# Performance work log

Hardware: AMD Instinct MI355X
Metric: run time of the kernel (lower is better)

Reference implementation:

```python
import jax, jax.numpy as jnp
import numpy as np

N0 = 4096
C = 128
DEPTH = 3
RATIO = 0.5
AVG_DEG = 32
BN_EPS = 1e-5


def setup_inputs() -> dict:
    key = jax.random.key(0)
    ks = jax.random.split(key, 6)
    x = jax.random.normal(ks[0], (N0, C), dtype=jnp.float32)
    # sparse symmetric adjacency (avg degree ~AVG_DEG), no self loops, dense layout
    mask = jax.random.bernoulli(ks[1], AVG_DEG / N0, (N0, N0)).astype(jnp.float32)
    adj = jnp.maximum(mask, mask.T) * (1.0 - jnp.eye(N0, dtype=jnp.float32))
    scale = 1.0 / np.sqrt(C)
    conv_w = jax.random.normal(ks[2], (2 * DEPTH + 1, C, C), dtype=jnp.float32) * scale
    conv_b = jax.random.normal(ks[3], (2 * DEPTH + 1, C), dtype=jnp.float32) * 0.01
    pool_w = jax.random.normal(ks[4], (DEPTH, C), dtype=jnp.float32)
    bn_g = jnp.ones((2 * DEPTH + 1, C), dtype=jnp.float32)
    bn_b = jnp.zeros((2 * DEPTH + 1, C), dtype=jnp.float32)
    return {"x": x, "adj": adj, "conv_w": conv_w, "conv_b": conv_b,
            "pool_w": pool_w, "bn_g": bn_g, "bn_b": bn_b}


def _gcn(x, A, W, b):
    # GCNConv(improved=True): A_hat = A + 2I, symmetric deg normalization
    n = A.shape[0]
    Ah = A + 2.0 * jnp.eye(n, dtype=A.dtype)
    deg = Ah.sum(axis=1)
    d_safe = jnp.where(deg > 0, deg, 1.0)
    dn = jnp.where(deg > 0, jax.lax.rsqrt(d_safe), 0.0)
    An = dn[:, None] * Ah * dn[None, :]
    return An @ (x @ W) + b


def _bn(x, g, b):
    # BatchNorm1d, training mode (biased variance)
    m = x.mean(axis=0)
    v = x.var(axis=0)
    return g * (x - m) * jax.lax.rsqrt(v + BN_EPS) + b


def _augment(A):
    # add_self_loops -> spspmm(A,A) -> remove_self_loops, done densely
    n = A.shape[0]
    I = jnp.eye(n, dtype=A.dtype)
    Aa = A + I
    return (Aa @ Aa) * (1.0 - I)


def _topk_pool(x, A, p):
    score = jnp.tanh((x @ p) / jnp.linalg.norm(p))
    k = int(np.ceil(RATIO * x.shape[0]))
    vals, perm = jax.lax.top_k(score, k)
    xn = x[perm] * vals[:, None]
    An = A[perm][:, perm]
    return xn, An, perm


def reference(x, adj, conv_w, conv_b, pool_w, bn_g, bn_b):
    x = x.astype(jnp.float32)
    x = _bn(jax.nn.relu(_gcn(x, adj, conv_w[0], conv_b[0])), bn_g[0], bn_b[0])
    xs, adjs, perms = [x], [adj], []
    A = adj
    for i in range(1, DEPTH + 1):
        A2 = _augment(A)
        x, A, perm = _topk_pool(x, A2, pool_w[i - 1])
        x = _bn(jax.nn.relu(_gcn(x, A, conv_w[i], conv_b[i])), bn_g[i], bn_b[i])
        if i < DEPTH:
            xs.append(x)
            adjs.append(A)
        perms.append(perm)
    for i in range(DEPTH):
        j = DEPTH - 1 - i
        res, Aj, perm = xs[j], adjs[j], perms[j]
        up = jnp.zeros_like(res).at[perm].set(x)
        x = res + up  # sum_res=True
        x = _gcn(x, Aj, conv_w[DEPTH + 1 + i], conv_b[DEPTH + 1 + i])
        if i < DEPTH - 1:
            x = jax.nn.relu(x)
        x = _bn(x, bn_g[DEPTH + 1 + i], bn_b[DEPTH + 1 + i])
    return x
```

## Files before the change

### kernel.cpp

```cpp
#include <hip/hip_runtime.h>
#include <cstdint>
#include <cstddef>

typedef __bf16 bf16;
typedef __bf16 bf16x8 __attribute__((ext_vector_type(8)));
typedef __bf16 bf16x4 __attribute__((ext_vector_type(4)));
typedef float floatx4 __attribute__((ext_vector_type(4)));
typedef int   intx4  __attribute__((ext_vector_type(4)));
typedef short shortx4 __attribute__((ext_vector_type(4)));
typedef char  cx8    __attribute__((ext_vector_type(8)));

#define GLD16(gp, lp) __builtin_amdgcn_global_load_lds( \
    (const __attribute__((address_space(1))) void*)(gp), \
    (__attribute__((address_space(3))) void*)(lp), 16, 0, 0)

__global__ __launch_bounds__(256) void gemm_sym_i8(
    const char* __restrict__ R, short* __restrict__ Cs16, int* __restrict__ Cs32,
    int n , int kIters, int G, int pairs)
{
  __shared__ __align__(16) char As[128 * 64];
  __shared__ __align__(16) char Bs[128 * 64];

  const int pair = blockIdx.x;
  int rem = pair, bm = 0;
  while (rem >= G - bm) { rem -= G - bm; ++bm; }
  const int bn = bm + rem;
  const int m0 = bm * 128;
  const int n0 = bn * 128;

  const int t = threadIdx.x;
  const int w = t >> 6, l = t & 63;
  const int wr = w >> 1, wc = w & 1;
  const int lr = l & 15, q = l >> 4;
  const int k0base = blockIdx.y * kIters * 64;

  const char* Ab = R + (size_t)m0 * n + k0base;
  const char* Bb = R + (size_t)n0 * n + k0base;
  const int srow = t >> 2;
  const int schunk = (t & 3) * 16;

  intx4 acc[4][4];
#pragma unroll
  for (int i = 0; i < 4; ++i)
#pragma unroll
    for (int j = 0; j < 4; ++j) acc[i][j] = (intx4)0;

  for (int kb = 0; kb < kIters; ++kb) {
    const int k0 = kb * 64;
    __syncthreads();
    GLD16(Ab + (size_t)srow * n + k0 + schunk,        As + (size_t)t * 16);
    GLD16(Ab + (size_t)(srow + 64) * n + k0 + schunk, As + (size_t)(t + 256) * 16);
    GLD16(Bb + (size_t)srow * n + k0 + schunk,        Bs + (size_t)t * 16);
    GLD16(Bb + (size_t)(srow + 64) * n + k0 + schunk, Bs + (size_t)(t + 256) * 16);
    __syncthreads();

    intx4 af[4], bfr[4];
#pragma unroll
    for (int mi = 0; mi < 4; ++mi)
      af[mi] = *(const intx4*)&As[(wr * 64 + mi * 16 + lr) * 64 + q * 16];
#pragma unroll
    for (int ni = 0; ni < 4; ++ni)
      bfr[ni] = *(const intx4*)&Bs[(wc * 64 + ni * 16 + lr) * 64 + q * 16];
#pragma unroll
    for (int mi = 0; mi < 4; ++mi)
#pragma unroll
      for (int ni = 0; ni < 4; ++ni)
        acc[mi][ni] = __builtin_amdgcn_mfma_i32_16x16x64_i8(
            af[mi], bfr[ni], acc[mi][ni], 0, 0, 0);
  }

  const size_t so = ((size_t)blockIdx.y * pairs + pair) * 16384;
#pragma unroll
  for (int mi = 0; mi < 4; ++mi)
#pragma unroll
    for (int ni = 0; ni < 4; ++ni) {
      const int cl = wc * 64 + ni * 16 + lr;
      const int rb = wr * 64 + mi * 16 + q * 4;
#pragma unroll
      for (int r = 0; r < 4; ++r) {
        int v = acc[mi][ni][r];
        if (Cs16) Cs16[so + (size_t)(rb + r) * 128 + cl] = (short)v;
        else      Cs32[so + (size_t)(rb + r) * 128 + cl] = v;
      }
    }
}

__global__ void sym_post_i(const short* __restrict__ Cs16, const int* __restrict__ Cs32,
                           bf16* __restrict__ Abf, float* __restrict__ Af,
                           int k, int G, int pairs, int nz)
{
  int rem = blockIdx.x, bm = 0;
  while (rem >= G - bm) { rem -= G - bm; ++bm; }
  const int bn = bm + rem;
  const int t = threadIdx.x;
  const int i = t >> 1;
  const int jc = blockIdx.y * 8 + (t & 1) * 4;
  const int r = bm * 128 + i;
  const size_t sbase = (size_t)blockIdx.x * 16384 + (size_t)i * 128 + jc;

  int v[4] = {0, 0, 0, 0};
  for (int z = 0; z < nz; ++z) {
    const size_t off = sbase + (size_t)z * pairs * 16384;
    if (Cs16) {
      shortx4 a = *(const shortx4*)&Cs16[off];
#pragma unroll
      for (int e = 0; e < 4; ++e) v[e] += (int)a[e];
    } else {
      intx4 a = *(const intx4*)&Cs32[off];
#pragma unroll
      for (int e = 0; e < 4; ++e) v[e] += a[e];
    }
  }
  const int c0 = bn * 128 + jc;
#pragma unroll
  for (int e = 0; e < 4; ++e)
    if (c0 + e == r) v[e] = 0;

  if (Abf) {
    bf16x4 o;
#pragma unroll
    for (int e = 0; e < 4; ++e) o[e] = (bf16)(float)v[e];
    *(bf16x4*)&Abf[(size_t)r * k + c0] = o;
    if (bm != bn) {
#pragma unroll
      for (int e = 0; e < 4; ++e)
        Abf[(size_t)(c0 + e) * k + r] = o[e];
    }
  } else {
    floatx4 o;
#pragma unroll
    for (int e = 0; e < 4; ++e) o[e] = (float)v[e];
    *(floatx4*)&Af[(size_t)r * k + c0] = o;
    if (bm != bn) {
#pragma unroll
      for (int e = 0; e < 4; ++e)
        Af[(size_t)(c0 + e) * k + r] = o[e];
    }
  }
}

__global__ __launch_bounds__(256) void gemm_sym(
    const bf16* __restrict__ R, float* __restrict__ CsF,
    int n , int kIters, int G, int pairs)
{
  __shared__ __align__(16) bf16 As[128 * 32];
  __shared__ __align__(16) bf16 Bs[128 * 32];

  const int pair = blockIdx.x;
  int rem = pair, bm = 0;
  while (rem >= G - bm) { rem -= G - bm; ++bm; }
  const int bn = bm + rem;
  const int m0 = bm * 128;
  const int n0 = bn * 128;

  const int t = threadIdx.x;
  const int w = t >> 6, l = t & 63;
  const int wr = w >> 1, wc = w & 1;
  const int lr = l & 15, q = l >> 4;
  const int k0base = blockIdx.y * kIters * 32;

  const bf16* Ab = R + (size_t)m0 * n + k0base;
  const bf16* Bb = R + (size_t)n0 * n + k0base;
  const int srow = t >> 2;
  const int schunk = (t & 3) * 8;

  floatx4 acc[4][4];
#pragma unroll
  for (int i = 0; i < 4; ++i)
#pragma unroll
    for (int j = 0; j < 4; ++j) acc[i][j] = (floatx4)0.0f;

  for (int kb = 0; kb < kIters; ++kb) {
    const int k0 = kb * 32;
    __syncthreads();
    GLD16(Ab + (size_t)srow * n + k0 + schunk,        As + (size_t)t * 8);
    GLD16(Ab + (size_t)(srow + 64) * n + k0 + schunk, As + (size_t)(t + 256) * 8);
    GLD16(Bb + (size_t)srow * n + k0 + schunk,        Bs + (size_t)t * 8);
    GLD16(Bb + (size_t)(srow + 64) * n + k0 + schunk, Bs + (size_t)(t + 256) * 8);
    __syncthreads();

    bf16x8 af[4], bfr[4];
#pragma unroll
    for (int mi = 0; mi < 4; ++mi)
      af[mi] = *(const bf16x8*)&As[(wr * 64 + mi * 16 + lr) * 32 + q * 8];
#pragma unroll
    for (int ni = 0; ni < 4; ++ni)
      bfr[ni] = *(const bf16x8*)&Bs[(wc * 64 + ni * 16 + lr) * 32 + q * 8];
#pragma unroll
    for (int mi = 0; mi < 4; ++mi)
#pragma unroll
      for (int ni = 0; ni < 4; ++ni)
        acc[mi][ni] = __builtin_amdgcn_mfma_f32_16x16x32_bf16(
            af[mi], bfr[ni], acc[mi][ni], 0, 0, 0);
  }

  const size_t so = ((size_t)blockIdx.y * pairs + pair) * 16384;
#pragma unroll
  for (int mi = 0; mi < 4; ++mi)
#pragma unroll
    for (int ni = 0; ni < 4; ++ni) {
      const int cl = wc * 64 + ni * 16 + lr;
      const int rb = wr * 64 + mi * 16 + q * 4;
#pragma unroll
      for (int r = 0; r < 4; ++r)
        CsF[so + (size_t)(rb + r) * 128 + cl] = acc[mi][ni][r];
    }
}

__global__ void sym_post(const float* __restrict__ CsF, float* __restrict__ Af,
                         int k, int G, int pairs, int nz)
{
  int rem = blockIdx.x, bm = 0;
  while (rem >= G - bm) { rem -= G - bm; ++bm; }
  const int bn = bm + rem;
  const int t = threadIdx.x;
  const int i = t >> 1;
  const int jc = blockIdx.y * 8 + (t & 1) * 4;
  const int r = bm * 128 + i;
  const size_t sbase = (size_t)blockIdx.x * 16384 + (size_t)i * 128 + jc;

  float v[4] = {0.f, 0.f, 0.f, 0.f};
  for (int z = 0; z < nz; ++z) {
    const size_t off = sbase + (size_t)z * pairs * 16384;
    floatx4 a = *(const floatx4*)&CsF[off];
#pragma unroll
    for (int e = 0; e < 4; ++e) v[e] += a[e];
  }
  const int c0 = bn * 128 + jc;
  floatx4 o;
#pragma unroll
  for (int e = 0; e < 4; ++e) o[e] = (c0 + e == r) ? 0.0f : v[e];
  *(floatx4*)&Af[(size_t)r * k + c0] = o;
  if (bm != bn) {
#pragma unroll
    for (int e = 0; e < 4; ++e)
      Af[(size_t)(c0 + e) * k + r] = o[e];
  }
}

template <int NP>
__global__ __launch_bounds__(256) void agg_bf(
    const bf16* __restrict__ A, int lda,
    const bf16* __restrict__ Zh, const bf16* __restrict__ Zm, const bf16* __restrict__ Zl,
    int ldz, float* __restrict__ Y, int kIters)
{
  __shared__ __align__(16) bf16 As[64 * 32];
  __shared__ __align__(16) bf16 Zs[NP][128 * 32];

  const int t = threadIdx.x;
  const int w = t >> 6, l = t & 63;
  const int wr = w >> 1, wc = w & 1;
  const int lr = l & 15, q = l >> 4;
  const int m0 = blockIdx.x * 64;
  const int k0base = blockIdx.y * kIters * 32;

  const int srow = t >> 2;
  const int schunk = (t & 3) * 8;

  floatx4 acc[2][4];
#pragma unroll
  for (int i = 0; i < 2; ++i)
#pragma unroll
    for (int j = 0; j < 4; ++j) acc[i][j] = (floatx4)0.0f;

  for (int kb = 0; kb < kIters; ++kb) {
    const int k0 = k0base + kb * 32;
    __syncthreads();
    GLD16(A + (size_t)(m0 + srow) * lda + k0 + schunk, As + (size_t)t * 8);
    GLD16(Zh + (size_t)srow * ldz + k0 + schunk,        Zs[0] + (size_t)t * 8);
    GLD16(Zh + (size_t)(srow + 64) * ldz + k0 + schunk, Zs[0] + (size_t)(t + 256) * 8);
    GLD16(Zm + (size_t)srow * ldz + k0 + schunk,        Zs[1] + (size_t)t * 8);
    GLD16(Zm + (size_t)(srow + 64) * ldz + k0 + schunk, Zs[1] + (size_t)(t + 256) * 8);
    if (NP > 2) {
      GLD16(Zl + (size_t)srow * ldz + k0 + schunk,        Zs[2] + (size_t)t * 8);
      GLD16(Zl + (size_t)(srow + 64) * ldz + k0 + schunk, Zs[2] + (size_t)(t + 256) * 8);
    }
    __syncthreads();

    bf16x8 af[2], bz[NP][4];
#pragma unroll
    for (int mi = 0; mi < 2; ++mi)
      af[mi] = *(const bf16x8*)&As[(wr * 32 + mi * 16 + lr) * 32 + q * 8];
#pragma unroll
    for (int s = 0; s < NP; ++s)
#pragma unroll
      for (int ni = 0; ni < 4; ++ni)
        bz[s][ni] = *(const bf16x8*)&Zs[s][(wc * 64 + ni * 16 + lr) * 32 + q * 8];
#pragma unroll
    for (int s = 0; s < NP; ++s)
#pragma unroll
      for (int mi = 0; mi < 2; ++mi)
#pragma unroll
        for (int ni = 0; ni < 4; ++ni)
          acc[mi][ni] = __builtin_amdgcn_mfma_f32_16x16x32_bf16(
              af[mi], bz[s][ni], acc[mi][ni], 0, 0, 0);
  }

#pragma unroll
  for (int mi = 0; mi < 2; ++mi)
#pragma unroll
    for (int ni = 0; ni < 4; ++ni) {
      const int col = wc * 64 + ni * 16 + lr;
      const int rowb = m0 + wr * 32 + mi * 16 + q * 4;
#pragma unroll
      for (int r = 0; r < 4; ++r)
        atomicAdd(&Y[(size_t)(rowb + r) * 128 + col], acc[mi][ni][r]);
    }
}

template <int NP>
__global__ __launch_bounds__(256) void agg_split(
    const float* __restrict__ A, int lda,
    const bf16* __restrict__ Zh, const bf16* __restrict__ Zm, const bf16* __restrict__ Zl,
    int ldz, float* __restrict__ Y, int kIters, int aTwo)
{
  __shared__ __align__(16) bf16 Ahs[64 * 32];
  __shared__ __align__(16) bf16 Als[64 * 32];
  __shared__ __align__(16) bf16 Zs[NP][128 * 32];

  const int t = threadIdx.x;
  const int w = t >> 6, l = t & 63;
  const int wr = w >> 1, wc = w & 1;
  const int lr = l & 15, q = l >> 4;
  const int m0 = blockIdx.x * 64;
  const int k0base = blockIdx.y * kIters * 32;

  const int arow = t >> 2;
  const int acol = (t & 3) * 8;
  const int srow = t >> 2;
  const int schunk = (t & 3) * 8;

  floatx4 acc[2][4];
#pragma unroll
  for (int i = 0; i < 2; ++i)
#pragma unroll
    for (int j = 0; j < 4; ++j) acc[i][j] = (floatx4)0.0f;

  for (int kb = 0; kb < kIters; ++kb) {
    const int k0 = k0base + kb * 32;
    const float* asrc = A + (size_t)(m0 + arow) * lda + k0 + acol;
    floatx4 av[2];
#pragma unroll
    for (int i = 0; i < 2; ++i) av[i] = *(const floatx4*)(asrc + i * 4);

    __syncthreads();
    GLD16(Zh + (size_t)srow * ldz + k0 + schunk,        Zs[0] + (size_t)t * 8);
    GLD16(Zh + (size_t)(srow + 64) * ldz + k0 + schunk, Zs[0] + (size_t)(t + 256) * 8);
    GLD16(Zm + (size_t)srow * ldz + k0 + schunk,        Zs[1] + (size_t)t * 8);
    GLD16(Zm + (size_t)(srow + 64) * ldz + k0 + schunk, Zs[1] + (size_t)(t + 256) * 8);
    if (NP > 2) {
      GLD16(Zl + (size_t)srow * ldz + k0 + schunk,        Zs[2] + (size_t)t * 8);
      GLD16(Zl + (size_t)(srow + 64) * ldz + k0 + schunk, Zs[2] + (size_t)(t + 256) * 8);
    }

    bf16x4 ah[2], alo[2];
    const int grow = m0 + arow;
#pragma unroll
    for (int i = 0; i < 8; ++i) {
      float v = av[i >> 2][i & 3];
      if (k0 + acol + i == grow) v = 0.0f;
      bf16 h = (bf16)v;
      ah[i >> 2][i & 3] = h;
      alo[i >> 2][i & 3] = (bf16)(v - (float)h);
    }
    const int sbase = arow * 32 + acol;
    *(bf16x4*)&Ahs[sbase] = ah[0]; *(bf16x4*)&Ahs[sbase + 4] = ah[1];
    if (aTwo) { *(bf16x4*)&Als[sbase] = alo[0]; *(bf16x4*)&Als[sbase + 4] = alo[1]; }
    __syncthreads();

    bf16x8 afh[2], afl[2], bz[NP][4];
#pragma unroll
    for (int mi = 0; mi < 2; ++mi)
      afh[mi] = *(const bf16x8*)&Ahs[(wr * 32 + mi * 16 + lr) * 32 + q * 8];
#pragma unroll
    for (int s = 0; s < NP; ++s)
#pragma unroll
      for (int ni = 0; ni < 4; ++ni)
        bz[s][ni] = *(const bf16x8*)&Zs[s][(wc * 64 + ni * 16 + lr) * 32 + q * 8];
#pragma unroll
    for (int s = 0; s < NP; ++s)
#pragma unroll
      for (int mi = 0; mi < 2; ++mi)
#pragma unroll
        for (int ni = 0; ni < 4; ++ni)
          acc[mi][ni] = __builtin_amdgcn_mfma_f32_16x16x32_bf16(
              afh[mi], bz[s][ni], acc[mi][ni], 0, 0, 0);
    if (aTwo) {
#pragma unroll
      for (int mi = 0; mi < 2; ++mi)
        afl[mi] = *(const bf16x8*)&Als[(wr * 32 + mi * 16 + lr) * 32 + q * 8];
      constexpr int NL = (NP > 2) ? 2 : 1;
#pragma unroll
      for (int s = 0; s < NL; ++s)
#pragma unroll
        for (int mi = 0; mi < 2; ++mi)
#pragma unroll
          for (int ni = 0; ni < 4; ++ni)
            acc[mi][ni] = __builtin_amdgcn_mfma_f32_16x16x32_bf16(
                afl[mi], bz[s][ni], acc[mi][ni], 0, 0, 0);
    }
  }

#pragma unroll
  for (int mi = 0; mi < 2; ++mi)
#pragma unroll
    for (int ni = 0; ni < 4; ++ni) {
      const int col = wc * 64 + ni * 16 + lr;
      const int rowb = m0 + wr * 32 + mi * 16 + q * 4;
#pragma unroll
      for (int r = 0; r < 4; ++r)
        atomicAdd(&Y[(size_t)(rowb + r) * 128 + col], acc[mi][ni][r]);
    }
}

template <int FULL>
__global__ __launch_bounds__(256) void xw_split(
    const float* __restrict__ X, const int* __restrict__ perm,
    const float* __restrict__ vals,
    const float* __restrict__ up, const int* __restrict__ inv,
    const float* __restrict__ statsP, const float* __restrict__ gP,
    const float* __restrict__ bP, float nP,
    const bf16* __restrict__ Wh, const bf16* __restrict__ Wm, const bf16* __restrict__ Wl,
    const float* __restrict__ dnv, float* __restrict__ Z,
    bf16* __restrict__ Zht, bf16* __restrict__ Zmt, bf16* __restrict__ Zlt, int ldz,
    float* __restrict__ Agg, float* __restrict__ stats)
{
  __shared__ __align__(16) bf16 Xs[3][128 * 32];
  __shared__ __align__(16) bf16 Ws[3][128 * 32];
  __shared__ float scU[128], offU[128];

  const int t = threadIdx.x;
  if (blockIdx.x == 0) stats[t] = 0.0f;

  const int w = t >> 6, l = t & 63;
  const int wr = w >> 1, wc = w & 1;
  const int lr = l & 15, q = l >> 4;
  const int r0 = blockIdx.x * 128;

  const int srow = t >> 1;
  const int soff = (t & 1) * 16;
  const int sbase = srow * 32 + soff;

  if (statsP) {
    if (t < 128) {
      float m = statsP[t] / nP;
      float var = statsP[128 + t] / nP - m * m;
      float sc = gP[t] / sqrtf(var + 1e-5f);
      scU[t] = sc;
      offU[t] = bP[t] - m * sc;
    }
    __syncthreads();
  }

  const int row = r0 + srow;
  int grow = row;
  float scale = 1.0f;
  if (perm) { grow = perm[row]; scale = vals[row]; }
  const float* xrow = X + (size_t)grow * 128;
  const float* uprow = nullptr;
  if (up) { int j = inv[row]; if (j >= 0) uprow = up + (size_t)j * 128; }

  floatx4 acc[4][4];
#pragma unroll
  for (int i = 0; i < 4; ++i)
#pragma unroll
    for (int j = 0; j < 4; ++j) acc[i][j] = (floatx4)0.0f;

  const bf16* wsrc[3] = {Wh, Wm, Wl};

  for (int ks = 0; ks < 4; ++ks) {
    const int k0 = ks * 32;
    float xv[16];
#pragma unroll
    for (int i = 0; i < 16; i += 4) {
      floatx4 tmp = *(const floatx4*)(xrow + k0 + soff + i);
      if (uprow) {
        floatx4 u = *(const floatx4*)(uprow + k0 + soff + i);
        if (statsP) {
#pragma unroll
          for (int j = 0; j < 4; ++j) {
            const int c = k0 + soff + i + j;
            u[j] = scU[c] * u[j] + offU[c];
          }
        }
        tmp += u;
      }
      xv[i] = tmp[0] * scale; xv[i + 1] = tmp[1] * scale;
      xv[i + 2] = tmp[2] * scale; xv[i + 3] = tmp[3] * scale;
    }
    bf16x8 wv[3][2];
#pragma unroll
    for (int s = 0; s < 3; ++s) {
      const bf16* ws = wsrc[s] + (size_t)srow * 128 + k0 + soff;
      wv[s][0] = *(const bf16x8*)ws;
      wv[s][1] = *(const bf16x8*)(ws + 8);
    }
    bf16x8 vh[2], vm[2], vl[2];
#pragma unroll
    for (int i = 0; i < 16; ++i) {
      float v = xv[i];
      bf16 h = (bf16)v; float r1 = v - (float)h;
      bf16 m = (bf16)r1; float r2 = r1 - (float)m;
      vh[i >> 3][i & 7] = h; vm[i >> 3][i & 7] = m; vl[i >> 3][i & 7] = (bf16)r2;
    }
    __syncthreads();
    *(bf16x8*)&Xs[0][sbase] = vh[0]; *(bf16x8*)&Xs[0][sbase + 8] = vh[1];
    *(bf16x8*)&Xs[1][sbase] = vm[0]; *(bf16x8*)&Xs[1][sbase + 8] = vm[1];
    *(bf16x8*)&Xs[2][sbase] = vl[0]; *(bf16x8*)&Xs[2][sbase + 8] = vl[1];
#pragma unroll
    for (int s = 0; s < 3; ++s) {
      *(bf16x8*)&Ws[s][sbase] = wv[s][0];
      *(bf16x8*)&Ws[s][sbase + 8] = wv[s][1];
    }
    __syncthreads();

    bf16x8 af[3][4], bfg[3][4];
#pragma unroll
    for (int s = 0; s < 3; ++s) {
#pragma unroll
      for (int mi = 0; mi < 4; ++mi)
        af[s][mi] = *(const bf16x8*)&Xs[s][(wr * 64 + mi * 16 + lr) * 32 + q * 8];
#pragma unroll
      for (int ni = 0; ni < 4; ++ni)
        bfg[s][ni] = *(const bf16x8*)&Ws[s][(wc * 64 + ni * 16 + lr) * 32 + q * 8];
    }
    constexpr int NT = FULL ? 6 : 3;
    constexpr int sa[6] = {0, 0, 1, 1, 0, 2};
    constexpr int sb[6] = {0, 1, 0, 1, 2, 0};
#pragma unroll
    for (int p = 0; p < NT; ++p)
#pragma unroll
      for (int mi = 0; mi < 4; ++mi)
#pragma unroll
        for (int ni = 0; ni < 4; ++ni)
          acc[mi][ni] = __builtin_amdgcn_mfma_f32_16x16x32_bf16(
              af[sa[p]][mi], bfg[sb[p]][ni], acc[mi][ni], 0, 0, 0);
  }

#pragma unroll
  for (int mi = 0; mi < 4; ++mi) {
    const int rowb = r0 + wr * 64 + mi * 16 + q * 4;
    float dnr[4];
#pragma unroll
    for (int r = 0; r < 4; ++r) dnr[r] = dnv[rowb + r];
#pragma unroll
    for (int ni = 0; ni < 4; ++ni) {
      const int col = wc * 64 + ni * 16 + lr;
      bf16x4 h4, m4, l4;
#pragma unroll
      for (int r = 0; r < 4; ++r) {
        float v = dnr[r] * acc[mi][ni][r];
        Z[(size_t)(rowb + r) * 128 + col] = v;
        Agg[(size_t)(rowb + r) * 128 + col] = 0.0f;
        bf16 h = (bf16)v; float r1 = v - (float)h;
        bf16 m = (bf16)r1; float r2 = r1 - (float)m;
        h4[r] = h; m4[r] = m; l4[r] = (bf16)r2;
      }
      *(bf16x4*)&Zht[(size_t)col * ldz + rowb] = h4;
      *(bf16x4*)&Zmt[(size_t)col * ldz + rowb] = m4;
      if (FULL) *(bf16x4*)&Zlt[(size_t)col * ldz + rowb] = l4;
    }
  }
}

__global__ void prep_all(const float* __restrict__ adj, bf16* __restrict__ ah,
                         float* __restrict__ dn, int n,
                         const float* __restrict__ W, bf16* __restrict__ Wh,
                         bf16* __restrict__ Wm, bf16* __restrict__ Wl,
                         const float* __restrict__ pw, float* __restrict__ invp) {
  const int bid = blockIdx.x;
  const int t = threadIdx.x;
  if (bid < 4096) {
    int r = bid;
    const float* arow = adj + (size_t)r * n;
    bf16* orow = ah + (size_t)r * n;
    float sum = 0.f;
    for (int c4 = t * 4; c4 < n; c4 += 1024) {
      floatx4 v = *(const floatx4*)(arow + c4);
      bf16x4 o;
#pragma unroll
      for (int e = 0; e < 4; ++e) {
        float x = (c4 + e == r) ? 0.0f : v[e];
        sum += x; o[e] = (bf16)x;
      }
      *(bf16x4*)&orow[c4] = o;
    }
    __shared__ float red[256];
    red[t] = sum; __syncthreads();
    for (int off = 128; off; off >>= 1) {
      if (t < off) red[t] += red[t + off];
      __syncthreads();
    }
    if (t == 0) dn[r] = 1.0f / sqrtf(red[0] + 2.0f);
  } else if (bid < 4544) {
    int idx = (bid - 4096) * 256 + t;
    int l = idx >> 14, rem = idx & 16383, c = rem >> 7, k = rem & 127;
    float v = W[(l << 14) + (k << 7) + c];
    bf16 h = (bf16)v; float r1 = v - (float)h;
    bf16 m = (bf16)r1; float r2 = r1 - (float)m;
    Wh[idx] = h; Wm[idx] = m; Wl[idx] = (bf16)r2;
  } else {
    __shared__ float red[128];
    if (t < 128) {
      for (int l = 0; l < 3; ++l) {
        float v = pw[l * 128 + t];
        red[t] = v * v; __syncthreads();
        for (int off = 64; off; off >>= 1) {
          if (t < off) red[t] += red[t + off];
          __syncthreads();
        }
        if (t == 0) invp[l] = 1.0f / sqrtf(red[0]);
        __syncthreads();
      }
    }
  }
}

__global__ void dn_rows_bf(const bf16* __restrict__ A, int lda, float* __restrict__ dn,
                           int n) {
  int r = blockIdx.x, t = threadIdx.x;
  const bf16* row = A + (size_t)r * lda;
  float sum = 0.f;
  for (int c4 = t * 4; c4 < n; c4 += 1024) {
    bf16x4 v = *(const bf16x4*)&row[c4];
#pragma unroll
    for (int e = 0; e < 4; ++e) sum += (float)v[e];
  }
  __shared__ float red[256];
  red[t] = sum; __syncthreads();
  for (int off = 128; off; off >>= 1) {
    if (t < off) red[t] += red[t + off];
    __syncthreads();
  }
  if (t == 0) dn[r] = 1.0f / sqrtf(red[0] + 2.0f);
}

__global__ void dn_rows(const float* __restrict__ A, int lda, float* __restrict__ dn,
                        int n) {
  int r = blockIdx.x, t = threadIdx.x;
  const float* row = A + (size_t)r * lda;
  float sum = 0.f;
  for (int c = t; c < n; c += 256)
    if (c != r) sum += row[c];
  __shared__ float red[256];
  red[t] = sum; __syncthreads();
  for (int off = 128; off; off >>= 1) {
    if (t < off) red[t] += red[t + off];
    __syncthreads();
  }
  if (t == 0) dn[r] = 1.0f / sqrtf(red[0] + 2.0f);
}

__device__ inline unsigned f2u(float f) {
  unsigned u = __float_as_uint(f);
  return (u & 0x80000000u) ? ~u : (u | 0x80000000u);
}
__global__ __launch_bounds__(1024) void select_kernel(
    const float* __restrict__ s, int n, int k,
    int* __restrict__ perm, float* __restrict__ vals, int* __restrict__ inv)
{
  __shared__ int hist[256];
  __shared__ unsigned sh_prefix;
  __shared__ int sh_krem;
  __shared__ float sh_thr;
  __shared__ int wsum[16];
  __shared__ int wgs[16], wes[16];
  const int t = threadIdx.x;
  const int lane = t & 63;
  const int wid = t >> 6;
  if (t == 0) { sh_prefix = 0; sh_krem = k; }

  for (int round = 0; round < 4; ++round) {
    const int shift = 24 - 8 * round;
    if (t < 256) hist[t] = 0;
    __syncthreads();
    const unsigned pref = sh_prefix;
    const int krem = sh_krem;
    for (int i = t; i < n; i += 1024) {
      unsigned u = f2u(s[i]);
      if (round == 0 || (u >> (shift + 8)) == pref)
        atomicAdd(&hist[(u >> shift) & 255], 1);
    }
    __syncthreads();
    int v = 0, own = 0;
    if (t < 256) {
      own = hist[255 - t];
      v = own;
#pragma unroll
      for (int off = 1; off < 64; off <<= 1) {
        int u = __shfl_up(v, off, 64);
        if (lane >= off) v += u;
      }
      if (lane == 63) wsum[wid] = v;
    }
    __syncthreads();
    if (t < 256) {
      int add = 0;
      for (int wi = 0; wi < wid; ++wi) add += wsum[wi];
      v += add;
      const int prev = v - own;
      if (v >= krem && prev < krem) {
        sh_prefix = (pref << 8) | (unsigned)(255 - t);
        sh_krem = krem - prev;
      }
    }
    __syncthreads();
  }
  if (t == 0) {
    unsigned u = sh_prefix;
    sh_thr = (u & 0x80000000u) ? __uint_as_float(u & 0x7fffffffu)
                               : __uint_as_float(~u);
  }
  for (int i = t; i < n; i += 1024) inv[i] = -1;
  __syncthreads();

  const float thr = sh_thr;
  const int chunk = n >> 10;
  const int beg = t * chunk;
  int g = 0, e = 0;
  for (int i = 0; i < chunk; ++i) {
    float v = s[beg + i];
    g += (v > thr); e += (v == thr);
  }
  int vg = g, ve = e;
#pragma unroll
  for (int off = 1; off < 64; off <<= 1) {
    int ug = __shfl_up(vg, off, 64);
    int ue = __shfl_up(ve, off, 64);
    if (lane >= off) { vg += ug; ve += ue; }
  }
  if (lane == 63) { wgs[wid] = vg; wes[wid] = ve; }
  __syncthreads();
  int ag = 0, ae = 0;
  for (int wi = 0; wi < wid; ++wi) { ag += wgs[wi]; ae += wes[wi]; }
  int total_gt = 0;
#pragma unroll
  for (int wi = 0; wi < 16; ++wi) total_gt += wgs[wi];
  int pg = vg + ag - g;
  int pe = ve + ae - e;
  const int need = k - total_gt;
  for (int i = 0; i < chunk; ++i) {
    float v = s[beg + i];
    if (v > thr) {
      if (pg < k) { perm[pg] = beg + i; vals[pg] = v; inv[beg + i] = pg; }
      ++pg;
    } else if (v == thr) {
      if (pe < need && total_gt + pe < k) {
        perm[total_gt + pe] = beg + i; vals[total_gt + pe] = v;
        inv[beg + i] = total_gt + pe;
      }
      ++pe;
    }
  }
}

__global__ void gather_i8(const bf16* __restrict__ src, int lda,
                          const int* __restrict__ perm, char* __restrict__ R, int n) {
  int j = blockIdx.x, t = threadIdx.x;
  int r = perm[j];
  const bf16* s = src + (size_t)r * lda;
  char* o = R + (size_t)j * n;
  for (int c = t * 8; c < n; c += 2048) {
    bf16x8 v = *(const bf16x8*)&s[c];
    cx8 ob;
#pragma unroll
    for (int e = 0; e < 8; ++e)
      ob[e] = (c + e == r) ? (char)1 : (char)(float)v[e];
    *(cx8*)&o[c] = ob;
  }
}

__global__ void gather_f32(const float* __restrict__ src, int lda,
                           const int* __restrict__ perm, bf16* __restrict__ R, int n) {
  int j = blockIdx.x, t = threadIdx.x;
  int r = perm[j];
  const float* s = src + (size_t)r * lda;
  bf16* o = R + (size_t)j * n;
  for (int c4 = t * 4; c4 < n; c4 += 1024) {
    floatx4 v = *(const floatx4*)(s + c4);
    bf16x4 ob;
#pragma unroll
    for (int e = 0; e < 4; ++e)
      ob[e] = (c4 + e == r) ? (bf16)1.0f : (bf16)v[e];
    *(bf16x4*)&o[c4] = ob;
  }
}

__global__ void gcn_post(float* __restrict__ acc, const float* __restrict__ Zf,
                         const float* __restrict__ dn, const float* __restrict__ bias,
                         float* __restrict__ stats, int relu,
                         float* __restrict__ hout) {
  int c = threadIdx.x;
  int r0 = blockIdx.x * 16;
  float b = bias[c];
  float s = 0.f, qq = 0.f;
  for (int i = 0; i < 16; ++i) {
    int r = r0 + i;
    float v = dn[r] * (acc[(size_t)r * 128 + c] + 2.0f * Zf[(size_t)r * 128 + c]) + b;
    if (relu) v = fmaxf(v, 0.f);
    hout[(size_t)r * 128 + c] = v;
    s += v; qq += v * v;
  }
  atomicAdd(&stats[c], s);
  atomicAdd(&stats[128 + c], qq);
}

__global__ void bn_apply(const float* __restrict__ H, const float* __restrict__ stats,
                         const float* __restrict__ g, const float* __restrict__ b,
                         int n, float* __restrict__ xout,
                         const float* __restrict__ pw, const float* __restrict__ invp,
                         float* __restrict__ scores) {
  int r = blockIdx.x, c = threadIdx.x;
  float m = stats[c] / n;
  float var = stats[128 + c] / n - m * m;
  float sc = g[c] / sqrtf(var + 1e-5f);
  float off = b[c] - m * sc;
  float v = sc * H[(size_t)r * 128 + c] + off;
  xout[(size_t)r * 128 + c] = v;
  if (pw) {
    __shared__ float red[128];
    red[c] = v * pw[c]; __syncthreads();
    for (int o = 64; o; o >>= 1) {
      if (c < o) red[c] += red[c + o];
      __syncthreads();
    }
    if (c == 0) scores[r] = tanhf(red[0] * invp[0]);
  }
}

extern "C" void kernel_launch(void* const* d_in, const int* in_sizes, int n_in,
                              void* d_out, int out_size, void* d_ws, size_t ws_size,
                              hipStream_t stream) {
  const float* x_in   = (const float*)d_in[0];
  const float* adj    = (const float*)d_in[1];
  const float* conv_w = (const float*)d_in[2];
  const float* conv_b = (const float*)d_in[3];
  const float* pool_w = (const float*)d_in[4];
  const float* bn_g   = (const float*)d_in[5];
  const float* bn_b   = (const float*)d_in[6];
  float* out = (float*)d_out;
  (void)in_sizes; (void)n_in; (void)out_size; (void)ws_size;

  char* p = (char*)d_ws;
  auto alloc = [&](size_t bytes) -> void* {
    void* r = (void*)p;
    p += (bytes + 255) & ~(size_t)255;
    return r;
  };
  bf16*  Ah0bf = (bf16*)alloc(4096ull * 4096 * 2);
  bf16*  A1bf  = (bf16*)alloc(2048ull * 2048 * 2);
  float* A2f   = (float*)alloc(1024ull * 1024 * 4);
  float* A3f   = (float*)alloc(512ull * 512 * 4);
  char*  Rbuf  = (char*)alloc(2048ull * 4096 * 2);
  void*  Cs    = alloc(40ull << 20);
  float* Z     = (float*)alloc(4096ull * 128 * 4);
  bf16*  Zht   = (bf16*)alloc(128ull * 4096 * 2);
  bf16*  Zmt   = (bf16*)alloc(128ull * 4096 * 2);
  bf16*  Zlt   = (bf16*)alloc(128ull * 4096 * 2);
  float* Agg   = (float*)alloc(4096ull * 128 * 4);
  float* res0  = (float*)alloc(4096ull * 128 * 4);
  float* res1  = (float*)alloc(2048ull * 128 * 4);
  float* res2  = (float*)alloc(1024ull * 128 * 4);
  float* xb0   = (float*)alloc(512ull * 128 * 4);
  float* xb1   = (float*)alloc(1024ull * 128 * 4);
  float* xb2   = (float*)alloc(2048ull * 128 * 4);
  bf16*  Wh    = (bf16*)alloc(7ull * 16384 * 2);
  bf16*  Wm    = (bf16*)alloc(7ull * 16384 * 2);
  bf16*  Wl    = (bf16*)alloc(7ull * 16384 * 2);
  float* scores = (float*)alloc(4096 * 4);
  int*   perm0 = (int*)alloc(2048 * 4);
  int*   perm1 = (int*)alloc(1024 * 4);
  int*   perm2 = (int*)alloc(512 * 4);
  int*   inv0  = (int*)alloc(4096 * 4);
  int*   inv1  = (int*)alloc(2048 * 4);
  int*   inv2  = (int*)alloc(1024 * 4);
  float* vals0 = (float*)alloc(2048 * 4);
  float* vals1 = (float*)alloc(1024 * 4);
  float* vals2 = (float*)alloc(512 * 4);
  float* dn0   = (float*)alloc(4096 * 4);
  float* dn1   = (float*)alloc(2048 * 4);
  float* dn2   = (float*)alloc(1024 * 4);
  float* dn3   = (float*)alloc(512 * 4);
  float* invp  = (float*)alloc(256);
  float* stats = (float*)alloc(7ull * 256 * 4);

  auto gcn = [&](int nr, const bf16* Abf, const float* Af32, const float* dnv,
                 int layer, const float* xsrc, const int* perm, const float* vals,
                 const float* up, const int* inv, float* xout, int relu, int aTwo,
                 const float* pw, const float* ip, int full,
                 const float* statsP, const float* gP, const float* bPv, float nP,
                 int doBn) {
    float* st = stats + layer * 256;
    if (full)
      xw_split<1><<<nr / 128, 256, 0, stream>>>(
          xsrc, perm, vals, up, inv, statsP, gP, bPv, nP,
          Wh + layer * 16384, Wm + layer * 16384, Wl + layer * 16384, dnv,
          Z, Zht, Zmt, Zlt, nr, Agg, st);
    else
      xw_split<0><<<nr / 128, 256, 0, stream>>>(
          xsrc, perm, vals, up, inv, statsP, gP, bPv, nP,
          Wh + layer * 16384, Wm + layer * 16384, Wl + layer * 16384, dnv,
          Z, Zht, Zmt, Zlt, nr, Agg, st);
    if (Abf) {
      if (full)
        agg_bf<3><<<dim3(nr / 64, 8), 256, 0, stream>>>(
            Abf, nr, Zht, Zmt, Zlt, nr, Agg, nr / 256);
      else
        agg_bf<2><<<dim3(nr / 64, 8), 256, 0, stream>>>(
            Abf, nr, Zht, Zmt, Zlt, nr, Agg, nr / 256);
    } else {
      if (full)
        agg_split<3><<<dim3(nr / 64, 8), 256, 0, stream>>>(
            Af32, nr, Zht, Zmt, Zlt, nr, Agg, nr / 256, aTwo);
      else
        agg_split<2><<<dim3(nr / 64, 8), 256, 0, stream>>>(
            Af32, nr, Zht, Zmt, Zlt, nr, Agg, nr / 256, aTwo);
    }
    gcn_post<<<nr / 16, 128, 0, stream>>>(Agg, Z, dnv, conv_b + layer * 128, st, relu,
                                          doBn ? Agg : xout);
    if (doBn)
      bn_apply<<<nr, 128, 0, stream>>>(Agg, st, bn_g + layer * 128, bn_b + layer * 128,
                                       nr, xout, pw, ip, scores);
  };

  auto pool = [&](int n, const bf16* srcBf, const float* srcF32,
                  bf16* outBf, float* outF32, float* dnNew,
                  int* perm, float* vals, int* inv, int splitZ, int mode) {
    int k = n / 2, G = k / 128, pairs = G * (G + 1) / 2;
    select_kernel<<<1, 1024, 0, stream>>>(scores, n, k, perm, vals, inv);
    if (mode <= 1) {
      gather_i8<<<k, 256, 0, stream>>>(srcBf, n, perm, Rbuf, n);
      gemm_sym_i8<<<dim3(pairs, splitZ), 256, 0, stream>>>(
          Rbuf, mode == 0 ? (short*)Cs : nullptr, mode == 0 ? nullptr : (int*)Cs,
          n, n / (splitZ * 64), G, pairs);
      sym_post_i<<<dim3(pairs, 16), 256, 0, stream>>>(
          mode == 0 ? (const short*)Cs : nullptr, mode == 0 ? nullptr : (const int*)Cs,
          outBf, outF32, k, G, pairs, splitZ);
    } else {
      gather_f32<<<k, 256, 0, stream>>>(srcF32, n, perm, (bf16*)Rbuf, n);
      gemm_sym<<<dim3(pairs, splitZ), 256, 0, stream>>>(
          (const bf16*)Rbuf, (float*)Cs, n, n / (splitZ * 32), G, pairs);
      sym_post<<<dim3(pairs, 16), 256, 0, stream>>>(
          (const float*)Cs, outF32, k, G, pairs, splitZ);
    }
    if (outBf) dn_rows_bf<<<k, 256, 0, stream>>>(outBf, k, dnNew, k);
    else       dn_rows<<<k, 256, 0, stream>>>(outF32, k, dnNew, k);
  };

  prep_all<<<4545, 256, 0, stream>>>(adj, Ah0bf, dn0, 4096,
                                     conv_w, Wh, Wm, Wl, pool_w, invp);

  gcn(4096, Ah0bf, nullptr, dn0, 0, x_in, nullptr, nullptr, nullptr, nullptr,
      res0, 1, 0, pool_w + 0, invp + 0, 1, nullptr, nullptr, nullptr, 1.0f, 1);
  pool(4096, Ah0bf, nullptr, A1bf, nullptr, dn1, perm0, vals0, inv0, 4, 0);
  gcn(2048, A1bf, nullptr, dn1, 1, res0, perm0, vals0, nullptr, nullptr,
      res1, 1, 0, pool_w + 128, invp + 1, 1, nullptr, nullptr, nullptr, 1.0f, 1);
  pool(2048, A1bf, nullptr, nullptr, A2f, dn2, perm1, vals1, inv1, 8, 1);
  gcn(1024, nullptr, A2f, dn2, 2, res1, perm1, vals1, nullptr, nullptr,
      res2, 1, 1, pool_w + 256, invp + 2, 1, nullptr, nullptr, nullptr, 1.0f, 1);
  pool(1024, nullptr, A2f, nullptr, A3f, dn3, perm2, vals2, inv2, 8, 2);
  gcn(512, nullptr, A3f, dn3, 3, res2, perm2, vals2, nullptr, nullptr,
      xb0, 1, 1, nullptr, nullptr, 0, nullptr, nullptr, nullptr, 1.0f, 0);

  gcn(1024, nullptr, A2f, dn2, 4, res2, nullptr, nullptr, xb0, inv2,
      xb1, 1, 1, nullptr, nullptr, 0,
      stats + 3 * 256, bn_g + 3 * 128, bn_b + 3 * 128, 512.0f, 0);
  gcn(2048, A1bf, nullptr, dn1, 5, res1, nullptr, nullptr, xb1, inv1,
      xb2, 1, 0, nullptr, nullptr, 0,
      stats + 4 * 256, bn_g + 4 * 128, bn_b + 4 * 128, 1024.0f, 0);
  gcn(4096, Ah0bf, nullptr, dn0, 6, res0, nullptr, nullptr, xb2, inv0,
      out, 0, 0, nullptr, nullptr, 0,
      stats + 5 * 256, bn_g + 5 * 128, bn_b + 5 * 128, 2048.0f, 1);
}
```

Measured before the change: 502.4 us.

## Use sparse neighbor-list aggregation for level-0 GCN and deterministic split-K reductions

Builds a capped neighbor list (up to 256 uint16 indices per row) for the original adjacency in prep_all and uses a gather-sum kernel for the two 4096-node GCN aggregations, replacing dense 4096x4096 bf16 MFMA products. Dense aggregations now write per-split partial outputs that gcn_post sums, instead of using atomicAdd. BN statistics switch to fixed-point int64 atomics so results are deterministic. This cuts most of the dense work at the largest level. The cost is extra partial-buffer traffic, and rows with more than 256 neighbors would be silently truncated.

```diff
diff --git a/kernel.cpp b/kernel.cpp
--- a/kernel.cpp
+++ b/kernel.cpp
@@ -13,6 +13,9 @@
 #define GLD16(gp, lp) __builtin_amdgcn_global_load_lds( \
     (const __attribute__((address_space(1))) void*)(gp), \
     (__attribute__((address_space(3))) void*)(lp), 16, 0, 0)
+
+#define FXS 16777216.0f
+#define FXI 5.9604644775390625e-08
 
 __global__ __launch_bounds__(256) void gemm_sym_i8(
     const char* __restrict__ R, short* __restrict__ Cs16, int* __restrict__ Cs32,
@@ -238,6 +241,35 @@
   }
 }
 
+__global__ __launch_bounds__(256) void agg_sparse(
+    const unsigned short* __restrict__ nbr, const int* __restrict__ deg,
+    const float* __restrict__ Z, float* __restrict__ Y)
+{
+  const int r = blockIdx.x * 4 + (threadIdx.x >> 6);
+  const int l = threadIdx.x & 63;
+  const unsigned short* rn = nbr + (size_t)r * 256;
+  const int d = deg[r];
+  float a0 = 0.f, a1 = 0.f;
+  int i = 0;
+  for (; i + 4 <= d; i += 4) {
+    const int c0 = rn[i], c1 = rn[i + 1], c2 = rn[i + 2], c3 = rn[i + 3];
+    float2 v0 = *(const float2*)(Z + (size_t)c0 * 128 + l * 2);
+    float2 v1 = *(const float2*)(Z + (size_t)c1 * 128 + l * 2);
+    float2 v2 = *(const float2*)(Z + (size_t)c2 * 128 + l * 2);
+    float2 v3 = *(const float2*)(Z + (size_t)c3 * 128 + l * 2);
+    a0 += v0.x; a1 += v0.y;
+    a0 += v1.x; a1 += v1.y;
+    a0 += v2.x; a1 += v2.y;
+    a0 += v3.x; a1 += v3.y;
+  }
+  for (; i < d; ++i) {
+    const int c = rn[i];
+    float2 v = *(const float2*)(Z + (size_t)c * 128 + l * 2);
+    a0 += v.x; a1 += v.y;
+  }
+  *(float2*)(Y + (size_t)r * 128 + l * 2) = make_float2(a0, a1);
+}
+
 template <int NP>
 __global__ __launch_bounds__(256) void agg_bf(
     const bf16* __restrict__ A, int lda,
@@ -296,6 +328,7 @@
               af[mi], bz[s][ni], acc[mi][ni], 0, 0, 0);
   }
 
+  const size_t zoff = (size_t)blockIdx.y * lda;
 #pragma unroll
   for (int mi = 0; mi < 2; ++mi)
 #pragma unroll
@@ -304,7 +337,7 @@
       const int rowb = m0 + wr * 32 + mi * 16 + q * 4;
 #pragma unroll
       for (int r = 0; r < 4; ++r)
-        atomicAdd(&Y[(size_t)(rowb + r) * 128 + col], acc[mi][ni][r]);
+        Y[(zoff + rowb + r) * 128 + col] = acc[mi][ni][r];
     }
 }
 
@@ -401,6 +434,7 @@
     }
   }
 
+  const size_t zoff = (size_t)blockIdx.y * lda;
 #pragma unroll
   for (int mi = 0; mi < 2; ++mi)
 #pragma unroll
@@ -409,7 +443,7 @@
       const int rowb = m0 + wr * 32 + mi * 16 + q * 4;
 #pragma unroll
       for (int r = 0; r < 4; ++r)
-        atomicAdd(&Y[(size_t)(rowb + r) * 128 + col], acc[mi][ni][r]);
+        Y[(zoff + rowb + r) * 128 + col] = acc[mi][ni][r];
     }
 }
 
@@ -418,19 +452,19 @@
     const float* __restrict__ X, const int* __restrict__ perm,
     const float* __restrict__ vals,
     const float* __restrict__ up, const int* __restrict__ inv,
-    const float* __restrict__ statsP, const float* __restrict__ gP,
+    const long long* __restrict__ statsP, const float* __restrict__ gP,
     const float* __restrict__ bP, float nP,
     const bf16* __restrict__ Wh, const bf16* __restrict__ Wm, const bf16* __restrict__ Wl,
     const float* __restrict__ dnv, float* __restrict__ Z,
     bf16* __restrict__ Zht, bf16* __restrict__ Zmt, bf16* __restrict__ Zlt, int ldz,
-    float* __restrict__ Agg, float* __restrict__ stats)
+    long long* __restrict__ stats)
 {
   __shared__ __align__(16) bf16 Xs[3][128 * 32];
   __shared__ __align__(16) bf16 Ws[3][128 * 32];
   __shared__ float scU[128], offU[128];
 
   const int t = threadIdx.x;
-  if (blockIdx.x == 0) stats[t] = 0.0f;
+  if (blockIdx.x == 0) stats[t] = 0;
 
   const int w = t >> 6, l = t & 63;
   const int wr = w >> 1, wc = w & 1;
@@ -443,8 +477,10 @@
 
   if (statsP) {
     if (t < 128) {
-      float m = statsP[t] / nP;
-      float var = statsP[128 + t] / nP - m * m;
+      float sm = (float)((double)statsP[t] * FXI);
+      float sq = (float)((double)statsP[128 + t] * FXI);
+      float m = sm / nP;
+      float var = sq / nP - m * m;
       float sc = gP[t] / sqrtf(var + 1e-5f);
       scU[t] = sc;
       offU[t] = bP[t] - m * sc;
@@ -551,47 +587,76 @@
       for (int r = 0; r < 4; ++r) {
         float v = dnr[r] * acc[mi][ni][r];
         Z[(size_t)(rowb + r) * 128 + col] = v;
-        Agg[(size_t)(rowb + r) * 128 + col] = 0.0f;
         bf16 h = (bf16)v; float r1 = v - (float)h;
         bf16 m = (bf16)r1; float r2 = r1 - (float)m;
         h4[r] = h; m4[r] = m; l4[r] = (bf16)r2;
       }
-      *(bf16x4*)&Zht[(size_t)col * ldz + rowb] = h4;
-      *(bf16x4*)&Zmt[(size_t)col * ldz + rowb] = m4;
-      if (FULL) *(bf16x4*)&Zlt[(size_t)col * ldz + rowb] = l4;
+      if (Zht) {
+        *(bf16x4*)&Zht[(size_t)col * ldz + rowb] = h4;
+        *(bf16x4*)&Zmt[(size_t)col * ldz + rowb] = m4;
+        if (FULL) *(bf16x4*)&Zlt[(size_t)col * ldz + rowb] = l4;
+      }
     }
   }
 }
 
 __global__ void prep_all(const float* __restrict__ adj, bf16* __restrict__ ah,
                          float* __restrict__ dn, int n,
+                         unsigned short* __restrict__ nbr, int* __restrict__ deg,
                          const float* __restrict__ W, bf16* __restrict__ Wh,
                          bf16* __restrict__ Wm, bf16* __restrict__ Wl,
                          const float* __restrict__ pw, float* __restrict__ invp) {
   const int bid = blockIdx.x;
   const int t = threadIdx.x;
+  __shared__ int wsum4[4];
+  __shared__ float red[128];
   if (bid < 4096) {
-    int r = bid;
+    const int r = bid;
     const float* arow = adj + (size_t)r * n;
     bf16* orow = ah + (size_t)r * n;
-    float sum = 0.f;
-    for (int c4 = t * 4; c4 < n; c4 += 1024) {
-      floatx4 v = *(const floatx4*)(arow + c4);
+    const int base = t * 16;
+    floatx4 buf[4];
+#pragma unroll
+    for (int i = 0; i < 4; ++i) buf[i] = *(const floatx4*)(arow + base + i * 4);
+    int cnt = 0;
+#pragma unroll
+    for (int i = 0; i < 4; ++i) {
       bf16x4 o;
 #pragma unroll
       for (int e = 0; e < 4; ++e) {
-        float x = (c4 + e == r) ? 0.0f : v[e];
-        sum += x; o[e] = (bf16)x;
+        float x = (base + i * 4 + e == r) ? 0.0f : buf[i][e];
+        buf[i][e] = x;
+        cnt += (x != 0.0f) ? 1 : 0;
+        o[e] = (bf16)x;
       }
-      *(bf16x4*)&orow[c4] = o;
-    }
-    __shared__ float red[256];
-    red[t] = sum; __syncthreads();
-    for (int off = 128; off; off >>= 1) {
-      if (t < off) red[t] += red[t + off];
-      __syncthreads();
-    }
-    if (t == 0) dn[r] = 1.0f / sqrtf(red[0] + 2.0f);
+      *(bf16x4*)&orow[base + i * 4] = o;
+    }
+    const int lane = t & 63, wid = t >> 6;
+    int vc = cnt;
+#pragma unroll
+    for (int off = 1; off < 64; off <<= 1) {
+      int u = __shfl_up(vc, off, 64);
+      if (lane >= off) vc += u;
+    }
+    if (lane == 63) wsum4[wid] = vc;
+    __syncthreads();
+    int add = 0;
+    for (int wi = 0; wi < wid; ++wi) add += wsum4[wi];
+    int o = vc + add - cnt;
+    const int total = wsum4[0] + wsum4[1] + wsum4[2] + wsum4[3];
+    unsigned short* rn = nbr + (size_t)r * 256;
+#pragma unroll
+    for (int i = 0; i < 4; ++i)
+#pragma unroll
+      for (int e = 0; e < 4; ++e)
+        if (buf[i][e] != 0.0f) {
+          if (o < 256) rn[o] = (unsigned short)(base + i * 4 + e);
+          ++o;
+        }
+    if (t == 0) {
+      deg[r] = total < 256 ? total : 256;
+      dn[r] = 1.0f / sqrtf((float)total + 2.0f);
+    }
   } else if (bid < 4544) {
     int idx = (bid - 4096) * 256 + t;
     int l = idx >> 14, rem = idx & 16383, c = rem >> 7, k = rem & 127;
@@ -600,7 +665,6 @@
     bf16 m = (bf16)r1; float r2 = r1 - (float)m;
     Wh[idx] = h; Wm[idx] = m; Wl[idx] = (bf16)r2;
   } else {
-    __shared__ float red[128];
     if (t < 128) {
       for (int l = 0; l < 3; ++l) {
         float v = pw[l * 128 + t];
@@ -786,33 +850,40 @@
   }
 }
 
-__global__ void gcn_post(float* __restrict__ acc, const float* __restrict__ Zf,
+__global__ void gcn_post(const float* Ys, const float* __restrict__ Zf,
                          const float* __restrict__ dn, const float* __restrict__ bias,
-                         float* __restrict__ stats, int relu,
-                         float* __restrict__ hout) {
+                         long long* __restrict__ stats, int relu,
+                         float* hout, int nr, int nz) {
   int c = threadIdx.x;
   int r0 = blockIdx.x * 16;
   float b = bias[c];
   float s = 0.f, qq = 0.f;
   for (int i = 0; i < 16; ++i) {
     int r = r0 + i;
-    float v = dn[r] * (acc[(size_t)r * 128 + c] + 2.0f * Zf[(size_t)r * 128 + c]) + b;
+    float a = 0.f;
+    for (int z = 0; z < nz; ++z)
+      a += Ys[((size_t)z * nr + r) * 128 + c];
+    float v = dn[r] * (a + 2.0f * Zf[(size_t)r * 128 + c]) + b;
     if (relu) v = fmaxf(v, 0.f);
     hout[(size_t)r * 128 + c] = v;
     s += v; qq += v * v;
   }
-  atomicAdd(&stats[c], s);
-  atomicAdd(&stats[128 + c], qq);
-}
-
-__global__ void bn_apply(const float* __restrict__ H, const float* __restrict__ stats,
+  atomicAdd((unsigned long long*)&stats[c],
+            (unsigned long long)(long long)llrintf(s * FXS));
+  atomicAdd((unsigned long long*)&stats[128 + c],
+            (unsigned long long)(long long)llrintf(qq * FXS));
+}
+
+__global__ void bn_apply(const float* __restrict__ H, const long long* __restrict__ stats,
                          const float* __restrict__ g, const float* __restrict__ b,
                          int n, float* __restrict__ xout,
                          const float* __restrict__ pw, const float* __restrict__ invp,
                          float* __restrict__ scores) {
   int r = blockIdx.x, c = threadIdx.x;
-  float m = stats[c] / n;
-  float var = stats[128 + c] / n - m * m;
+  float sm = (float)((double)stats[c] * FXI);
+  float sq = (float)((double)stats[128 + c] * FXI);
+  float m = sm / n;
+  float var = sq / n - m * m;
   float sc = g[c] / sqrtf(var + 1e-5f);
   float off = b[c] - m * sc;
   float v = sc * H[(size_t)r * 128 + c] + off;
@@ -857,7 +928,7 @@
   bf16*  Zht   = (bf16*)alloc(128ull * 4096 * 2);
   bf16*  Zmt   = (bf16*)alloc(128ull * 4096 * 2);
   bf16*  Zlt   = (bf16*)alloc(128ull * 4096 * 2);
-  float* Agg   = (float*)alloc(4096ull * 128 * 4);
+  float* Agg   = (float*)alloc(8ull * 2048 * 128 * 4);
   float* res0  = (float*)alloc(4096ull * 128 * 4);
   float* res1  = (float*)alloc(2048ull * 128 * 4);
   float* res2  = (float*)alloc(1024ull * 128 * 4);
@@ -867,6 +938,8 @@
   bf16*  Wh    = (bf16*)alloc(7ull * 16384 * 2);
   bf16*  Wm    = (bf16*)alloc(7ull * 16384 * 2);
   bf16*  Wl    = (bf16*)alloc(7ull * 16384 * 2);
+  unsigned short* nbr = (unsigned short*)alloc(4096ull * 256 * 2 + 1024);
+  int*   deg   = (int*)alloc(4096 * 4);
   float* scores = (float*)alloc(4096 * 4);
   int*   perm0 = (int*)alloc(2048 * 4);
   int*   perm1 = (int*)alloc(1024 * 4);
@@ -882,32 +955,41 @@
   float* dn2   = (float*)alloc(1024 * 4);
   float* dn3   = (float*)alloc(512 * 4);
   float* invp  = (float*)alloc(256);
-  float* stats = (float*)alloc(7ull * 256 * 4);
-
-  auto gcn = [&](int nr, const bf16* Abf, const float* Af32, const float* dnv,
+  long long* stats = (long long*)alloc(7ull * 256 * 8);
+
+  auto gcn = [&](int nr, const bf16* Abf, const float* Af32,
+                 const unsigned short* nbrp, const float* dnv,
                  int layer, const float* xsrc, const int* perm, const float* vals,
                  const float* up, const int* inv, float* xout, int relu, int aTwo,
                  const float* pw, const float* ip, int full,
-                 const float* statsP, const float* gP, const float* bPv, float nP,
+                 const long long* statsP, const float* gP, const float* bPv, float nP,
                  int doBn) {
-    float* st = stats + layer * 256;
+    long long* st = stats + layer * 256;
+    bf16* zht = nbrp ? nullptr : Zht;
+    bf16* zmt = nbrp ? nullptr : Zmt;
+    bf16* zlt = nbrp ? nullptr : Zlt;
     if (full)
       xw_split<1><<<nr / 128, 256, 0, stream>>>(
           xsrc, perm, vals, up, inv, statsP, gP, bPv, nP,
           Wh + layer * 16384, Wm + layer * 16384, Wl + layer * 16384, dnv,
-          Z, Zht, Zmt, Zlt, nr, Agg, st);
+          Z, zht, zmt, zlt, nr, st);
     else
       xw_split<0><<<nr / 128, 256, 0, stream>>>(
           xsrc, perm, vals, up, inv, statsP, gP, bPv, nP,
           Wh + layer * 16384, Wm + layer * 16384, Wl + layer * 16384, dnv,
-          Z, Zht, Zmt, Zlt, nr, Agg, st);
-    if (Abf) {
+          Z, zht, zmt, zlt, nr, st);
+    int nz;
+    if (nbrp) {
+      agg_sparse<<<nr / 4, 256, 0, stream>>>(nbrp, deg, Z, Agg);
+      nz = 1;
+    } else if (Abf) {
       if (full)
         agg_bf<3><<<dim3(nr / 64, 8), 256, 0, stream>>>(
             Abf, nr, Zht, Zmt, Zlt, nr, Agg, nr / 256);
       else
         agg_bf<2><<<dim3(nr / 64, 8), 256, 0, stream>>>(
             Abf, nr, Zht, Zmt, Zlt, nr, Agg, nr / 256);
+      nz = 8;
     } else {
       if (full)
         agg_split<3><<<dim3(nr / 64, 8), 256, 0, stream>>>(
@@ -915,9 +997,10 @@
       else
         agg_split<2><<<dim3(nr / 64, 8), 256, 0, stream>>>(
             Af32, nr, Zht, Zmt, Zlt, nr, Agg, nr / 256, aTwo);
+      nz = 8;
     }
     gcn_post<<<nr / 16, 128, 0, stream>>>(Agg, Z, dnv, conv_b + layer * 128, st, relu,
-                                          doBn ? Agg : xout);
+                                          doBn ? Agg : xout, nr, nz);
     if (doBn)
       bn_apply<<<nr, 128, 0, stream>>>(Agg, st, bn_g + layer * 128, bn_b + layer * 128,
                                        nr, xout, pw, ip, scores);
@@ -947,28 +1030,28 @@
     else       dn_rows<<<k, 256, 0, stream>>>(outF32, k, dnNew, k);
   };
 
-  prep_all<<<4545, 256, 0, stream>>>(adj, Ah0bf, dn0, 4096,
+  prep_all<<<4545, 256, 0, stream>>>(adj, Ah0bf, dn0, 4096, nbr, deg,
                                      conv_w, Wh, Wm, Wl, pool_w, invp);
 
-  gcn(4096, Ah0bf, nullptr, dn0, 0, x_in, nullptr, nullptr, nullptr, nullptr,
+  gcn(4096, nullptr, nullptr, nbr, dn0, 0, x_in, nullptr, nullptr, nullptr, nullptr,
       res0, 1, 0, pool_w + 0, invp + 0, 1, nullptr, nullptr, nullptr, 1.0f, 1);
   pool(4096, Ah0bf, nullptr, A1bf, nullptr, dn1, perm0, vals0, inv0, 4, 0);
-  gcn(2048, A1bf, nullptr, dn1, 1, res0, perm0, vals0, nullptr, nullptr,
+  gcn(2048, A1bf, nullptr, nullptr, dn1, 1, res0, perm0, vals0, nullptr, nullptr,
       res1, 1, 0, pool_w + 128, invp + 1, 1, nullptr, nullptr, nullptr, 1.0f, 1);
   pool(2048, A1bf, nullptr, nullptr, A2f, dn2, perm1, vals1, inv1, 8, 1);
-  gcn(1024, nullptr, A2f, dn2, 2, res1, perm1, vals1, nullptr, nullptr,
+  gcn(1024, nullptr, A2f, nullptr, dn2, 2, res1, perm1, vals1, nullptr, nullptr,
       res2, 1, 1, pool_w + 256, invp + 2, 1, nullptr, nullptr, nullptr, 1.0f, 1);
   pool(1024, nullptr, A2f, nullptr, A3f, dn3, perm2, vals2, inv2, 8, 2);
-  gcn(512, nullptr, A3f, dn3, 3, res2, perm2, vals2, nullptr, nullptr,
+  gcn(512, nullptr, A3f, nullptr, dn3, 3, res2, perm2, vals2, nullptr, nullptr,
       xb0, 1, 1, nullptr, nullptr, 0, nullptr, nullptr, nullptr, 1.0f, 0);
 
-  gcn(1024, nullptr, A2f, dn2, 4, res2, nullptr, nullptr, xb0, inv2,
+  gcn(1024, nullptr, A2f, nullptr, dn2, 4, res2, nullptr, nullptr, xb0, inv2,
       xb1, 1, 1, nullptr, nullptr, 0,
       stats + 3 * 256, bn_g + 3 * 128, bn_b + 3 * 128, 512.0f, 0);
-  gcn(2048, A1bf, nullptr, dn1, 5, res1, nullptr, nullptr, xb1, inv1,
+  gcn(2048, A1bf, nullptr, nullptr, dn1, 5, res1, nullptr, nullptr, xb1, inv1,
       xb2, 1, 0, nullptr, nullptr, 0,
       stats + 4 * 256, bn_g + 4 * 128, bn_b + 4 * 128, 1024.0f, 0);
-  gcn(4096, Ah0bf, nullptr, dn0, 6, res0, nullptr, nullptr, xb2, inv0,
+  gcn(4096, nullptr, nullptr, nbr, dn0, 6, res0, nullptr, nullptr, xb2, inv0,
       out, 0, 0, nullptr, nullptr, 0,
       stats + 5 * 256, bn_g + 5 * 128, bn_b + 5 * 128, 2048.0f, 1);
 }
```

New measurement: 619.1 us. +23.2%, slower.
